# Kernel tuning notes

Measured on AMD Instinct MI355X. Metric: run time of the kernel, lower is better.

## Reference

```python
import jax, jax.numpy as jnp
import numpy as np

B, T, D, H, E, O = 4, 2048, 512, 2048, 4, 512
C = 1024  # expert capacity
HE = H // E  # per-expert hidden width


def setup_inputs() -> dict:
    key = jax.random.key(0)
    ks = jax.random.split(key, 7)
    x = jax.random.normal(ks[0], (B, T, D), dtype=jnp.float32)
    dispatch_mask = jax.random.uniform(ks[1], (B, T, E, C), dtype=jnp.float32)
    combine_array = jax.random.uniform(ks[2], (B, T, E, C), dtype=jnp.float32)
    # per-expert parameters (fc1 contract, fc2 expand)
    w1 = jax.random.normal(ks[3], (E, D, HE), dtype=jnp.float32) * (1.0 / np.sqrt(D))
    b1 = jnp.zeros((E, HE), dtype=jnp.float32)
    w2 = jax.random.normal(ks[4], (E, HE, O), dtype=jnp.float32) * (1.0 / np.sqrt(HE))
    b2 = jnp.zeros((O,), dtype=jnp.float32)
    return {"x": x, "dispatch_mask": dispatch_mask, "combine_array": combine_array,
            "w1": w1, "b1": b1, "w2": w2, "b2": b2}


def reference(x, dispatch_mask, combine_array, w1, b1, w2, b2):
    # dispatch: gather tokens into per-expert capacity buffers [B,E,C,D]
    xd = jnp.einsum('btd,btec->becd', x, dispatch_mask)
    # per-expert fc1: [B,E,C,HE]
    h = jnp.einsum('becd,edh->bech', xd, w1) + b1[None, :, None, :]
    # GELU (exact erf form, matching torch nn.GELU default); norm/dropout are identity
    h = jax.nn.gelu(h, approximate=False)
    # per-expert fc2: [B,E,C,O]
    y = jnp.einsum('bech,eho->beco', h, w2)
    # combine: scatter expert outputs back to tokens [B,T,O]
    out = jnp.einsum('beco,btec->bto', y, combine_array) + b2
    return out
```

## Files before the change

kernel.cpp:

```cpp
#include <hip/hip_runtime.h>
#include <math.h>

namespace {

typedef short short8 __attribute__((ext_vector_type(8)));
typedef int i32x4 __attribute__((ext_vector_type(4)));
typedef float f32x4 __attribute__((ext_vector_type(4)));

constexpr int kB = 4, kT = 2048, kD = 512, kE = 4, kC = 1024, kHE = 512,
              kO = 512, kEC = 4096;

__device__ __forceinline__ unsigned short f2bf(float f) {
    unsigned int u = __float_as_uint(f);
    u += 0x7fffu + ((u >> 16) & 1u);
    return (unsigned short)(u >> 16);
}

__device__ __forceinline__ float gelu_exact(float v) {
    return 0.5f * v * (1.0f + erff(v * 0.70710678118654752f));
}

#define GLDS16(g, l)                                                      \
    __builtin_amdgcn_global_load_lds(                                     \
        (const __attribute__((address_space(1))) unsigned int*)(g),       \
        (__attribute__((address_space(3))) unsigned int*)(l), 16, 0, 0)

__global__ __launch_bounds__(256)
void transpose_cast(const float* __restrict__ in, unsigned short* __restrict__ out,
                    int R, int Cc, long long sIn, long long sOut)
{
    __shared__ float tile[64][33];
    const int z = blockIdx.z;
    const float* ip = in + (long long)z * sIn;
    unsigned short* op = out + (long long)z * sOut;
    const int c0 = blockIdx.x * 32, r0 = blockIdx.y * 64;
    const int tx = threadIdx.x & 31, ty = threadIdx.x >> 5;
#pragma unroll
    for (int i = 0; i < 8; ++i) {
        const int r = ty + i * 8;
        tile[r][tx] = ip[(size_t)(r0 + r) * Cc + c0 + tx];
    }
    __syncthreads();
#pragma unroll
    for (int i = 0; i < 4; ++i) {
        const int c = ty + i * 8;
        const unsigned lo = f2bf(tile[tx * 2][c]);
        const unsigned hi = f2bf(tile[tx * 2 + 1][c]);
        *(unsigned*)&op[(size_t)(c0 + c) * R + r0 + tx * 2] = lo | (hi << 16);
    }
}

__global__ __launch_bounds__(256)
void cast_bf16(const float* __restrict__ in, unsigned short* __restrict__ out,
               long long n)
{
    const long long i = ((long long)blockIdx.x * blockDim.x + threadIdx.x) * 4;
    if (i < n) {
        const float4 v = *(const float4*)&in[i];
        unsigned short o[4] = {f2bf(v.x), f2bf(v.y), f2bf(v.z), f2bf(v.w)};
        *(uint2*)&out[i] = *(const uint2*)o;
    }
}

template <int MODE>
__global__ __launch_bounds__(256, 2)
void mfma_gemm(const unsigned short* __restrict__ Aall,
               const unsigned short* __restrict__ Ball,
               const float* __restrict__ biasAll,
               void* __restrict__ Call,
               int M, int N, int K,
               long long sA, long long sB, long long sC,
               int zModA, int zModB, int zModBias, int biasStride, int bShift)
{
    __shared__ unsigned short As[2][128 * 64];
    __shared__ unsigned short Bs[2][128 * 64];

    const int z = blockIdx.z;
    const unsigned short* Ab = Aall + (long long)(z % zModA) * sA;
    const unsigned short* Bb = Ball + (long long)(z % zModB) * sB;
    const float* bias =
        (MODE != 0) ? biasAll + (long long)(z % zModBias) * biasStride : nullptr;

    const int gx = gridDim.x;
    int lin = blockIdx.y * gx + blockIdx.x;
    const int nwg = gx * gridDim.y;
    if ((nwg & 7) == 0) {
        const int q = nwg >> 3;
        lin = (lin & 7) * q + (lin >> 3);
    }
    const int gxs = 31 - __clz(gx);
    const int bx = lin & (gx - 1);
    const int by = lin >> gxs;
    const int row0 = by * 128;
    const int colB = bx * 128;

    const int t = threadIdx.x;
    const int lane = t & 63;
    const int w = t >> 6;
    const int wrow = w * 32;
    const int l8r = lane >> 3;
    const int l8c = ((lane & 7) ^ l8r) * 8;

    const int wm = (w >> 1) * 64;
    const int wn = (w & 1) * 64;
    const int fr = lane & 15;
    const int fq = (lane >> 4) * 8;
    const int fsw = (fr & 7) * 8;

    const unsigned int bMask = (1u << bShift) - 1u;

    f32x4 acc[4][4] = {};

    const unsigned aB0 =
        (unsigned)(size_t)(const __attribute__((address_space(3))) unsigned short*)
            &As[0][0] +
        (unsigned)(((wm + fr) * 64 + (fq ^ fsw)) * 2);
    const unsigned bB0 =
        (unsigned)(size_t)(const __attribute__((address_space(3))) unsigned short*)
            &Bs[0][0] +
        (unsigned)(((wn + fr) * 64 + (fq ^ fsw)) * 2);

    struct FragSet { i32x4 a0[4], a1[4], b0[4], b1[4]; };
    FragSet R0, R1;

#define DSR0(d, a) asm volatile("ds_read_b128 %0, %1" : "=v"(d) : "v"(a))
#define DSR1(d, a) asm volatile("ds_read_b128 %0, %1 offset:2048" : "=v"(d) : "v"(a))
#define DSR2(d, a) asm volatile("ds_read_b128 %0, %1 offset:4096" : "=v"(d) : "v"(a))
#define DSR3(d, a) asm volatile("ds_read_b128 %0, %1 offset:6144" : "=v"(d) : "v"(a))

#define READ16(R, CB)                                                         \
    do {                                                                      \
        const unsigned A0c = aB0 + (CB) * 16384u, A1c = A0c ^ 64u;            \
        const unsigned B0c = bB0 + (CB) * 16384u, B1c = B0c ^ 64u;            \
        DSR0(R.a0[0], A0c); DSR1(R.a0[1], A0c); DSR2(R.a0[2], A0c); DSR3(R.a0[3], A0c); \
        DSR0(R.b0[0], B0c); DSR1(R.b0[1], B0c); DSR2(R.b0[2], B0c); DSR3(R.b0[3], B0c); \
        DSR0(R.a1[0], A1c); DSR1(R.a1[1], A1c); DSR2(R.a1[2], A1c); DSR3(R.a1[3], A1c); \
        DSR0(R.b1[0], B1c); DSR1(R.b1[1], B1c); DSR2(R.b1[2], B1c); DSR3(R.b1[3], B1c); \
    } while (0)

#define MFMA16(R)                                                             \
    do {                                                                      \
        _Pragma("unroll") for (int i_ = 0; i_ < 4; ++i_)                      \
            _Pragma("unroll") for (int j_ = 0; j_ < 4; ++j_)                  \
                acc[i_][j_] = __builtin_amdgcn_mfma_f32_16x16x32_bf16(        \
                    __builtin_bit_cast(short8, R.a0[i_]),                     \
                    __builtin_bit_cast(short8, R.b0[j_]), acc[i_][j_], 0, 0, 0); \
        _Pragma("unroll") for (int i_ = 0; i_ < 4; ++i_)                      \
            _Pragma("unroll") for (int j_ = 0; j_ < 4; ++j_)                  \
                acc[i_][j_] = __builtin_amdgcn_mfma_f32_16x16x32_bf16(        \
                    __builtin_bit_cast(short8, R.a1[i_]),                     \
                    __builtin_bit_cast(short8, R.b1[j_]), acc[i_][j_], 0, 0, 0); \
    } while (0)

#define STAGE(buf, k0)                                                        \
    do {                                                                      \
        _Pragma("unroll")                                                     \
        for (int r = 0; r < 4; ++r) {                                         \
            const int ar = row0 + wrow + r * 8 + l8r;                         \
            GLDS16(Ab + (size_t)ar * K + ((k0) + l8c),                        \
                   &As[buf][(wrow + r * 8) * 64]);                            \
            const int bn = colB + wrow + r * 8 + l8r;                         \
            const int gk = (k0) + l8c;                                        \
            const size_t boff =                                               \
                (((size_t)(gk >> bShift) * N + bn) << bShift) + (gk & bMask); \
            GLDS16(Bb + boff, &Bs[buf][(wrow + r * 8) * 64]);                 \
        }                                                                     \
    } while (0)

#define ITER_FULL(T, Rmf, Rrd)                                                \
    do {                                                                      \
        asm volatile("s_waitcnt vmcnt(0)" ::: "memory");                      \
        __builtin_amdgcn_s_barrier();                                         \
        STAGE((T) & 1, ((T) + 2) * 64);                                       \
        READ16(Rrd, ((T) + 1) & 1);                                           \
        MFMA16(Rmf);                                                          \
        asm volatile("s_waitcnt lgkmcnt(0)" ::: "memory");                    \
        __builtin_amdgcn_sched_barrier(0);                                    \
    } while (0)

    const int nt = K / 64;

    STAGE(0, 0);
    STAGE(1, 64);
    asm volatile("s_waitcnt vmcnt(8)" ::: "memory");
    __builtin_amdgcn_s_barrier();
    READ16(R0, 0);
    asm volatile("s_waitcnt lgkmcnt(0)" ::: "memory");
    __builtin_amdgcn_sched_barrier(0);

    for (int t0 = 0; t0 < nt - 2; t0 += 2) {
        ITER_FULL(t0 + 0, R0, R1);
        ITER_FULL(t0 + 1, R1, R0);
    }
    asm volatile("s_waitcnt vmcnt(0)" ::: "memory");
    __builtin_amdgcn_s_barrier();
    READ16(R1, (nt - 1) & 1);
    MFMA16(R0);
    asm volatile("s_waitcnt lgkmcnt(0)" ::: "memory");
    __builtin_amdgcn_sched_barrier(0);
    MFMA16(R1);

#undef ITER_FULL
#undef STAGE
#undef MFMA16
#undef READ16
#undef DSR0
#undef DSR1
#undef DSR2
#undef DSR3

    const long long cz = (long long)z * sC;
#pragma unroll
    for (int i = 0; i < 4; ++i) {
        const int rowb = row0 + wm + i * 16 + (lane >> 4) * 4;
#pragma unroll
        for (int j = 0; j < 4; ++j) {
            const int col = colB + wn + j * 16 + fr;
            const float bv = (MODE != 0) ? bias[col] : 0.0f;
#pragma unroll
            for (int r = 0; r < 4; ++r) {
                const float v = acc[i][j][r];
                const size_t idx = (size_t)cz + (size_t)(rowb + r) * N + col;
                if (MODE == 0)
                    ((unsigned short*)Call)[idx] = f2bf(v);
                else if (MODE == 1)
                    ((unsigned short*)Call)[idx] = f2bf(gelu_exact(v + bv));
                else
                    ((float*)Call)[idx] = v + bv;
            }
        }
    }
}

}

extern "C" void kernel_launch(void* const* d_in, const int* in_sizes, int n_in,
                              void* d_out, int out_size, void* d_ws, size_t ws_size,
                              hipStream_t stream)
{
    const float* x    = (const float*)d_in[0];
    const float* mask = (const float*)d_in[1];
    const float* comb = (const float*)d_in[2];
    const float* w1   = (const float*)d_in[3];
    const float* b1   = (const float*)d_in[4];
    const float* w2   = (const float*)d_in[5];
    const float* b2   = (const float*)d_in[6];
    float* out = (float*)d_out;

    unsigned short* ws    = (unsigned short*)d_ws;
    unsigned short* regA  = ws;
    unsigned short* xT    = regA + 33554432;
    unsigned short* w1T   = xT + 4194304;
    unsigned short* w2T   = w1T + 1048576;
    unsigned short* xd    = w2T + 1048576;
    unsigned short* h     = xd + 8388608;
    unsigned short* maskT = regA;
    unsigned short* combB = regA;
    unsigned short* yT    = xd;

    dim3 blk(256);

    transpose_cast<<<dim3(kEC / 32, kT / 64, kB), blk, 0, stream>>>(
        mask, maskT, kT, kEC, (long long)kT * kEC, (long long)kT * kEC);
    transpose_cast<<<dim3(kD / 32, kT / 64, kB), blk, 0, stream>>>(
        x, xT, kT, kD, (long long)kT * kD, (long long)kT * kD);
    transpose_cast<<<dim3(kHE / 32, kD / 64, kE), blk, 0, stream>>>(
        w1, w1T, kD, kHE, (long long)kD * kHE, (long long)kD * kHE);
    transpose_cast<<<dim3(kO / 32, kHE / 64, kE), blk, 0, stream>>>(
        w2, w2T, kHE, kO, (long long)kHE * kO, (long long)kHE * kO);

    mfma_gemm<0><<<dim3(kD / 128, kEC / 128, kB), blk, 0, stream>>>(
        maskT, xT, nullptr, xd, kEC, kD, kT,
        (long long)kEC * kT, (long long)kD * kT, (long long)kEC * kD,
        kB, kB, 1, 0, 11);

    cast_bf16<<<dim3(33554432 / 4 / 256), blk, 0, stream>>>(
        comb, combB, 33554432LL);

    mfma_gemm<1><<<dim3(kHE / 128, kC / 128, kB * kE), blk, 0, stream>>>(
        xd, w1T, b1, h, kC, kHE, kD,
        (long long)kC * kD, (long long)kHE * kD, (long long)kC * kHE,
        kB * kE, kE, kE, kHE, 9);

    mfma_gemm<0><<<dim3(kC / 128, kO / 128, kB * kE), blk, 0, stream>>>(
        w2T, h, nullptr, yT, kO, kC, kHE,
        (long long)kO * kHE, (long long)kC * kHE, (long long)kO * kC,
        kE, kB * kE, 1, 0, 9);

    mfma_gemm<3><<<dim3(kO / 128, kT / 128, kB), blk, 0, stream>>>(
        combB, yT, b2, out, kT, kO, kEC,
        (long long)kT * kEC, (long long)kE * kO * kC, (long long)kT * kO,
        kB, kB, 1, 0, 10);
}
```

Measured before the change: 426.6 us.

## Split-K the combine GEMM with atomic accumulation and reorder transpose grid

```diff
diff --git a/kernel.cpp b/kernel.cpp
--- a/kernel.cpp
+++ b/kernel.cpp
@@ -33,7 +33,7 @@
     const int z = blockIdx.z;
     const float* ip = in + (long long)z * sIn;
     unsigned short* op = out + (long long)z * sOut;
-    const int c0 = blockIdx.x * 32, r0 = blockIdx.y * 64;
+    const int r0 = blockIdx.x * 64, c0 = blockIdx.y * 32;
     const int tx = threadIdx.x & 31, ty = threadIdx.x >> 5;
 #pragma unroll
     for (int i = 0; i < 8; ++i) {
@@ -51,14 +51,19 @@
 }
 
 __global__ __launch_bounds__(256)
-void cast_bf16(const float* __restrict__ in, unsigned short* __restrict__ out,
-               long long n)
+void cast_and_zero(const float* __restrict__ in, unsigned short* __restrict__ out,
+                   int castBlocks, float* __restrict__ zbuf)
 {
-    const long long i = ((long long)blockIdx.x * blockDim.x + threadIdx.x) * 4;
-    if (i < n) {
+    const int bid = blockIdx.x;
+    if (bid < castBlocks) {
+        const long long i = ((long long)bid * blockDim.x + threadIdx.x) * 4;
         const float4 v = *(const float4*)&in[i];
         unsigned short o[4] = {f2bf(v.x), f2bf(v.y), f2bf(v.z), f2bf(v.w)};
         *(uint2*)&out[i] = *(const uint2*)o;
+    } else {
+        const long long i =
+            ((long long)(bid - castBlocks) * blockDim.x + threadIdx.x) * 4;
+        *(float4*)&zbuf[i] = make_float4(0.f, 0.f, 0.f, 0.f);
     }
 }
 
@@ -68,7 +73,7 @@
                const unsigned short* __restrict__ Ball,
                const float* __restrict__ biasAll,
                void* __restrict__ Call,
-               int M, int N, int K,
+               int M, int N, int K, int Kfull,
                long long sA, long long sB, long long sC,
                int zModA, int zModB, int zModBias, int biasStride, int bShift)
 {
@@ -80,6 +85,7 @@
     const unsigned short* Bb = Ball + (long long)(z % zModB) * sB;
     const float* bias =
         (MODE != 0) ? biasAll + (long long)(z % zModBias) * biasStride : nullptr;
+    const int kOff = (MODE == 4) ? (z / zModA) * K : 0;
 
     const int gx = gridDim.x;
     int lin = blockIdx.y * gx + blockIdx.x;
@@ -157,10 +163,10 @@
         _Pragma("unroll")                                                     \
         for (int r = 0; r < 4; ++r) {                                         \
             const int ar = row0 + wrow + r * 8 + l8r;                         \
-            GLDS16(Ab + (size_t)ar * K + ((k0) + l8c),                        \
+            GLDS16(Ab + (size_t)ar * Kfull + (kOff + (k0) + l8c),             \
                    &As[buf][(wrow + r * 8) * 64]);                            \
             const int bn = colB + wrow + r * 8 + l8r;                         \
-            const int gk = (k0) + l8c;                                        \
+            const int gk = kOff + (k0) + l8c;                                 \
             const size_t boff =                                               \
                 (((size_t)(gk >> bShift) * N + bn) << bShift) + (gk & bMask); \
             GLDS16(Bb + boff, &Bs[buf][(wrow + r * 8) * 64]);                 \
@@ -209,7 +215,7 @@
 #undef DSR2
 #undef DSR3
 
-    const long long cz = (long long)z * sC;
+    const long long cz = (long long)((MODE == 4) ? (z % zModA) : z) * sC;
 #pragma unroll
     for (int i = 0; i < 4; ++i) {
         const int rowb = row0 + wm + i * 16 + (lane >> 4) * 4;
@@ -225,8 +231,11 @@
                     ((unsigned short*)Call)[idx] = f2bf(v);
                 else if (MODE == 1)
                     ((unsigned short*)Call)[idx] = f2bf(gelu_exact(v + bv));
+                else if (MODE == 3)
+                    ((float*)Call)[idx] = v + bv;
                 else
-                    ((float*)Call)[idx] = v + bv;
+                    atomicAdd(&((float*)Call)[idx],
+                              v + ((z < zModA) ? bv : 0.0f));
             }
         }
     }
@@ -260,35 +269,35 @@
 
     dim3 blk(256);
 
-    transpose_cast<<<dim3(kEC / 32, kT / 64, kB), blk, 0, stream>>>(
+    transpose_cast<<<dim3(kT / 64, kEC / 32, kB), blk, 0, stream>>>(
         mask, maskT, kT, kEC, (long long)kT * kEC, (long long)kT * kEC);
-    transpose_cast<<<dim3(kD / 32, kT / 64, kB), blk, 0, stream>>>(
+    transpose_cast<<<dim3(kT / 64, kD / 32, kB), blk, 0, stream>>>(
         x, xT, kT, kD, (long long)kT * kD, (long long)kT * kD);
-    transpose_cast<<<dim3(kHE / 32, kD / 64, kE), blk, 0, stream>>>(
+    transpose_cast<<<dim3(kD / 64, kHE / 32, kE), blk, 0, stream>>>(
         w1, w1T, kD, kHE, (long long)kD * kHE, (long long)kD * kHE);
-    transpose_cast<<<dim3(kO / 32, kHE / 64, kE), blk, 0, stream>>>(
+    transpose_cast<<<dim3(kHE / 64, kO / 32, kE), blk, 0, stream>>>(
         w2, w2T, kHE, kO, (long long)kHE * kO, (long long)kHE * kO);
 
     mfma_gemm<0><<<dim3(kD / 128, kEC / 128, kB), blk, 0, stream>>>(
-        maskT, xT, nullptr, xd, kEC, kD, kT,
+        maskT, xT, nullptr, xd, kEC, kD, kT, kT,
         (long long)kEC * kT, (long long)kD * kT, (long long)kEC * kD,
         kB, kB, 1, 0, 11);
 
-    cast_bf16<<<dim3(33554432 / 4 / 256), blk, 0, stream>>>(
-        comb, combB, 33554432LL);
+    cast_and_zero<<<dim3(32768 + 4096), blk, 0, stream>>>(
+        comb, combB, 32768, out);
 
     mfma_gemm<1><<<dim3(kHE / 128, kC / 128, kB * kE), blk, 0, stream>>>(
-        xd, w1T, b1, h, kC, kHE, kD,
+        xd, w1T, b1, h, kC, kHE, kD, kD,
         (long long)kC * kD, (long long)kHE * kD, (long long)kC * kHE,
         kB * kE, kE, kE, kHE, 9);
 
     mfma_gemm<0><<<dim3(kC / 128, kO / 128, kB * kE), blk, 0, stream>>>(
-        w2T, h, nullptr, yT, kO, kC, kHE,
+        w2T, h, nullptr, yT, kO, kC, kHE, kHE,
         (long long)kO * kHE, (long long)kC * kHE, (long long)kO * kC,
         kE, kB * kE, 1, 0, 9);
 
-    mfma_gemm<3><<<dim3(kO / 128, kT / 128, kB), blk, 0, stream>>>(
-        combB, yT, b2, out, kT, kO, kEC,
+    mfma_gemm<4><<<dim3(kO / 128, kT / 128, kB * 2), blk, 0, stream>>>(
+        combB, yT, b2, out, kT, kO, kEC / 2, kEC,
         (long long)kT * kEC, (long long)kE * kO * kC, (long long)kT * kO,
         kB, kB, 1, 0, 10);
 }
```

Result: slower. 436.7 us (+2.4%).
